# Kernel tuning notes

Hardware: AMD Instinct MI355X
Metric: run time of the kernel (lower is better)

Reference implementation:

```python
import jax, jax.numpy as jnp
import numpy as np

D = 1024
H = 16

def setup_inputs() -> dict:
    key = jax.random.key(0)
    ks = jax.random.split(key, 5)
    x = jax.random.normal(ks[0], (4, 2048, D), dtype=jnp.float32)
    lim = 1.0 / np.sqrt(D)
    W_qkv = jax.random.uniform(ks[1], (D, 3 * D), minval=-lim, maxval=lim, dtype=jnp.float32)
    b_qkv = jax.random.uniform(ks[2], (3 * D,), minval=-lim, maxval=lim, dtype=jnp.float32)
    W_proj = jax.random.uniform(ks[3], (D, D), minval=-lim, maxval=lim, dtype=jnp.float32)
    b_proj = jax.random.uniform(ks[4], (D,), minval=-lim, maxval=lim, dtype=jnp.float32)
    return {"x": x, "W_qkv": W_qkv, "b_qkv": b_qkv, "W_proj": W_proj, "b_proj": b_proj}

def reference(x, W_qkv, b_qkv, W_proj, b_proj):
    B, T, d = x.shape
    hd = d // H
    scale = hd ** (-0.5)
    qkv = x @ W_qkv + b_qkv                       # [B,T,3D]
    qkv = qkv.reshape(B, T, 3, H, hd)
    q = qkv[:, :, 0].transpose(0, 2, 1, 3)        # [B,H,T,hd]
    k = qkv[:, :, 1].transpose(0, 2, 1, 3)
    v = qkv[:, :, 2].transpose(0, 2, 1, 3)
    scores = jnp.einsum('bhqd,bhkd->bhqk', q, k) * scale
    attn = jax.nn.softmax(scores, axis=-1)
    y = jnp.einsum('bhqk,bhkd->bhqd', attn, v)    # [B,H,T,hd]
    y = y.transpose(0, 2, 1, 3).reshape(B, T, d)
    return y @ W_proj + b_proj
```

## Files before the change

### kernel.cpp

```cpp
#include <hip/hip_runtime.h>


typedef __attribute__((ext_vector_type(8))) short bf16x8;
typedef __attribute__((ext_vector_type(8))) unsigned short u16x8;
typedef __attribute__((ext_vector_type(4))) float f32x4;
typedef __attribute__((ext_vector_type(16))) float f32x16;

#define DEV static __device__ __forceinline__

DEV unsigned short f2b(float f) {
  union { float f; unsigned int i; } v; v.f = f;
  unsigned int x = v.i;
  return (unsigned short)((x + 0x7FFFu + ((x >> 16) & 1u)) >> 16);
}

DEV f32x4 mfma16(bf16x8 a, bf16x8 b, f32x4 c) {
  return __builtin_amdgcn_mfma_f32_16x16x32_bf16(a, b, c, 0, 0, 0);
}
DEV f32x16 mfma32(bf16x8 a, bf16x8 b, f32x16 c) {
  return __builtin_amdgcn_mfma_f32_32x32x16_bf16(a, b, c, 0, 0, 0);
}

DEV void gl_lds16(const unsigned short* g, unsigned short* l) {
  __builtin_amdgcn_global_load_lds(
      (const __attribute__((address_space(1))) unsigned int*)g,
      (__attribute__((address_space(3))) unsigned int*)l, 16, 0, 0);
}

DEV void pk_swap(float a0, float a1, float b0, float b1,
                 unsigned int& w_lo, unsigned int& w_hi) {
  unsigned int a, b;
  asm("v_cvt_pk_bf16_f32 %0, %1, %2" : "=v"(a) : "v"(a0), "v"(a1));
  asm("v_cvt_pk_bf16_f32 %0, %1, %2" : "=v"(b) : "v"(b0), "v"(b1));
  asm("v_permlane32_swap_b32 %0, %1" : "+v"(a), "+v"(b));
  w_lo = a; w_hi = b;
}

__global__ __launch_bounds__(256) void prep(
    const float* __restrict__ x, unsigned short* __restrict__ xbf,
    const float* __restrict__ Wqkv, unsigned short* __restrict__ WqkvT,
    const float* __restrict__ Wproj, unsigned short* __restrict__ WprojT) {
  const int bid = blockIdx.x;
  if (bid < 8192) {
    const int i = (bid * 256 + threadIdx.x) * 4;
    const float4 v = *(const float4*)(x + i);
    ushort4 o;
    o.x = f2b(v.x); o.y = f2b(v.y); o.z = f2b(v.z); o.w = f2b(v.w);
    *(ushort4*)(xbf + i) = o;
    return;
  }
  __shared__ float tile[32][33];
  const float* in; unsigned short* out; int C, bx, by;
  if (bid < 11264) {
    const int bb = bid - 8192;
    bx = bb % 96; by = bb / 96; in = Wqkv; out = WqkvT; C = 3072;
  } else {
    const int bb = bid - 11264;
    bx = bb % 32; by = bb / 32; in = Wproj; out = WprojT; C = 1024;
  }
  const int R = 1024;
  const int tx = threadIdx.x & 31, ty = threadIdx.x >> 5;
  const int c0 = bx * 32, r0 = by * 32;
#pragma unroll
  for (int i = 0; i < 32; i += 8)
    tile[ty + i][tx] = in[(size_t)(r0 + ty + i) * C + (c0 + tx)];
  __syncthreads();
#pragma unroll
  for (int i = 0; i < 32; i += 8)
    out[(size_t)(c0 + ty + i) * R + (r0 + tx)] = f2b(tile[tx][ty + i]);
}

#define QSCALE 0.18033688f
template <int MODE>
__global__ __launch_bounds__(256, 2) void gemm_bt(
    const unsigned short* __restrict__ A, const unsigned short* __restrict__ Bt,
    const float* __restrict__ bias, void* __restrict__ out_v,
    int M, int N, int K) {
  __shared__ __align__(16) unsigned short As[128 * 64];
  __shared__ __align__(16) unsigned short Bs[128 * 64];
  const int tid = threadIdx.x;
  const int w = tid >> 6, l = tid & 63, g = l >> 4, ln = l & 15;
  const int wm = (w & 1) * 64, wn = (w >> 1) * 64;

  const int nwg = gridDim.x * gridDim.y;
  int wg = blockIdx.y * gridDim.x + blockIdx.x;
  wg = (wg & 7) * (nwg >> 3) + (wg >> 3);
  const int m0 = (wg / gridDim.x) * 128, n0 = (wg % gridDim.x) * 128;

  f32x4 acc[4][4];
#pragma unroll
  for (int i = 0; i < 4; ++i)
#pragma unroll
    for (int j = 0; j < 4; ++j) acc[i][j] = (f32x4){0.f, 0.f, 0.f, 0.f};

  const unsigned short* Ab = A + (size_t)m0 * K;
  const unsigned short* Bb = Bt + (size_t)n0 * K;
  const int lx = ln & 7;

  for (int k0 = 0; k0 < K; k0 += 64) {
#pragma unroll
    for (int i = 0; i < 4; ++i) {
      const int ch = tid + i * 256;
      const int ar = ch >> 3, s = ch & 7;
      const int sc = (s ^ (ar & 7)) * 8;
      gl_lds16(Ab + (size_t)ar * K + k0 + sc, &As[ch * 8]);
      gl_lds16(Bb + (size_t)ar * K + k0 + sc, &Bs[ch * 8]);
    }
    __syncthreads();
#pragma unroll
    for (int ks = 0; ks < 2; ++ks) {
      const int so = ((ks * 4 + g) ^ lx) * 8;
      bf16x8 af[4], bf[4];
#pragma unroll
      for (int mi = 0; mi < 4; ++mi)
        af[mi] = *(const bf16x8*)&As[(wm + mi * 16 + ln) * 64 + so];
#pragma unroll
      for (int ni = 0; ni < 4; ++ni)
        bf[ni] = *(const bf16x8*)&Bs[(wn + ni * 16 + ln) * 64 + so];
#pragma unroll
      for (int mi = 0; mi < 4; ++mi)
#pragma unroll
        for (int ni = 0; ni < 4; ++ni)
          acc[mi][ni] = mfma16(af[mi], bf[ni], acc[mi][ni]);
    }
    __syncthreads();
  }

#pragma unroll
  for (int mi = 0; mi < 4; ++mi) {
#pragma unroll
    for (int ni = 0; ni < 4; ++ni) {
      const int row0 = m0 + wm + mi * 16 + 4 * g;
      const int col = n0 + wn + ni * 16 + ln;
      const float bv = bias[col];
      if (MODE == 0) {
        const int which = col >> 10;
        const int h = (col >> 6) & 15;
        const int dd = col & 63;
        const int b = row0 >> 11, t0 = row0 & 2047;
        if (which == 2) {
          unsigned short* dst = (unsigned short*)out_v + (size_t)3 * 8388608u;
          ushort4 o;
          o.x = f2b(acc[mi][ni][0] + bv);
          o.y = f2b(acc[mi][ni][1] + bv);
          o.z = f2b(acc[mi][ni][2] + bv);
          o.w = f2b(acc[mi][ni][3] + bv);
          *(ushort4*)&dst[(((size_t)(b * 16 + h)) * 64 + dd) * 2048 + t0] = o;
        } else {
          unsigned short* dst = (unsigned short*)out_v + (size_t)which * 8388608u;
#pragma unroll
          for (int r = 0; r < 4; ++r) {
            float v = acc[mi][ni][r] + bv;
            if (which == 0) v *= QSCALE;
            dst[(((size_t)(b * 16 + h)) * 2048 + t0 + r) * 64 + dd] = f2b(v);
          }
        }
      } else {
#pragma unroll
        for (int r = 0; r < 4; ++r)
          ((float*)out_v)[(size_t)(row0 + r) * N + col] = acc[mi][ni][r] + bv;
      }
    }
  }
}

__global__ __launch_bounds__(256, 2) void attn(
    const unsigned short* __restrict__ Q, const unsigned short* __restrict__ K,
    const unsigned short* __restrict__ Vtg, unsigned short* __restrict__ Y) {
  __shared__ __align__(16) unsigned short Qs[128 * 72];
  __shared__ __align__(16) unsigned short Ks[64 * 72];
  __shared__ __align__(16) unsigned short Vt[64 * 72];

  const int tid = threadIdx.x;
  const int w = tid >> 6, l = tid & 63;
  const int l32 = l & 31, lh = l >> 5;
  const int wg = blockIdx.y * 16 + blockIdx.x;
  const int swz = (wg & 7) * 128 + (wg >> 3);
  const int bh = swz >> 4;
  const int q0 = (swz & 15) * 128;

  const unsigned short* Qb = Q + (size_t)bh * 131072;
  const unsigned short* Kb = K + (size_t)bh * 131072;
  const unsigned short* Vb = Vtg + (size_t)bh * 131072;

#pragma unroll
  for (int i = 0; i < 4; ++i) {
    const int c = tid + i * 256;
    u16x8 v = *(const u16x8*)(Qb + (size_t)q0 * 64 + c * 8);
    *(u16x8*)&Qs[(c >> 3) * 72 + (c & 7) * 8] = v;
  }
  __syncthreads();
  bf16x8 aq[4];
#pragma unroll
  for (int kb = 0; kb < 4; ++kb)
    aq[kb] = *(const bf16x8*)&Qs[(w * 32 + l32) * 72 + kb * 16 + lh * 8];

  const short one_b = (short)0x3F80;
  const bf16x8 vones = (bf16x8){one_b, one_b, one_b, one_b,
                                one_b, one_b, one_b, one_b};

  f32x16 o[2], os;
#pragma unroll
  for (int db = 0; db < 2; ++db)
#pragma unroll
    for (int r = 0; r < 16; ++r) o[db][r] = 0.f;
#pragma unroll
  for (int r = 0; r < 16; ++r) os[r] = 0.f;

  for (int kt = 0; kt < 32; ++kt) {
#pragma unroll
    for (int i = 0; i < 2; ++i) {
      const int c = tid + i * 256;
      const int row = c >> 3, cc = (c & 7) * 8;
      u16x8 kv = *(const u16x8*)(Kb + (size_t)kt * 4096 + c * 8);
      u16x8 vv = *(const u16x8*)(Vb + (size_t)row * 2048 + kt * 64 + cc);
      *(u16x8*)&Ks[row * 72 + cc] = kv;
      *(u16x8*)&Vt[row * 72 + cc] = vv;
    }
    __syncthreads();

    f32x16 s[2];
#pragma unroll
    for (int nb = 0; nb < 2; ++nb) {
#pragma unroll
      for (int r = 0; r < 16; ++r) s[nb][r] = 0.f;
#pragma unroll
      for (int kb = 0; kb < 4; ++kb) {
        bf16x8 bk = *(const bf16x8*)&Ks[(nb * 32 + l32) * 72 + kb * 16 + lh * 8];
        s[nb] = mfma32(bk, aq[kb], s[nb]);
      }
    }

    bf16x8 ap[4];
#pragma unroll
    for (int nb = 0; nb < 2; ++nb) {
      float pe[16];
#pragma unroll
      for (int r = 0; r < 16; ++r)
        pe[r] = __builtin_amdgcn_exp2f(s[nb][r]);
      union { unsigned int wd[4]; bf16x8 v; } u0, u1;
      pk_swap(pe[0], pe[1], pe[4], pe[5], u0.wd[0], u0.wd[2]);
      pk_swap(pe[2], pe[3], pe[6], pe[7], u0.wd[1], u0.wd[3]);
      pk_swap(pe[8], pe[9], pe[12], pe[13], u1.wd[0], u1.wd[2]);
      pk_swap(pe[10], pe[11], pe[14], pe[15], u1.wd[1], u1.wd[3]);
      ap[2 * nb + 0] = u0.v;
      ap[2 * nb + 1] = u1.v;
    }

#pragma unroll
    for (int ks = 0; ks < 4; ++ks) {
      os = mfma32(ap[ks], vones, os);
#pragma unroll
      for (int db = 0; db < 2; ++db) {
        bf16x8 bv = *(const bf16x8*)&Vt[(db * 32 + l32) * 72 + ks * 16 + lh * 8];
        o[db] = mfma32(ap[ks], bv, o[db]);
      }
    }
    __syncthreads();
  }

  float iv[16];
#pragma unroll
  for (int r = 0; r < 16; ++r) iv[r] = 1.f / os[r];

  const int b = bh >> 4, h = bh & 15;
#pragma unroll
  for (int db = 0; db < 2; ++db)
#pragma unroll
    for (int r = 0; r < 16; ++r) {
      const int row = (r & 3) + 8 * (r >> 2) + 4 * lh;
      const int t = q0 + w * 32 + row;
      Y[(size_t)(b * 2048 + t) * 1024 + h * 64 + db * 32 + l32] =
          f2b(o[db][r] * iv[r]);
    }
}

extern "C" void kernel_launch(void* const* d_in, const int* in_sizes, int n_in,
                              void* d_out, int out_size, void* d_ws, size_t ws_size,
                              hipStream_t stream) {
  const float* x     = (const float*)d_in[0];
  const float* Wqkv  = (const float*)d_in[1];
  const float* bqkv  = (const float*)d_in[2];
  const float* Wproj = (const float*)d_in[3];
  const float* bproj = (const float*)d_in[4];
  float* out = (float*)d_out;
  unsigned short* ws = (unsigned short*)d_ws;

  unsigned short* xbf    = ws;
  unsigned short* Yw     = xbf;
  unsigned short* WqkvT  = xbf + 8388608;
  unsigned short* WprojT = WqkvT + 3072 * 1024;
  unsigned short* Qw     = WprojT + 1024 * 1024;
  unsigned short* Kw     = Qw + 8388608;
  unsigned short* Vw     = Kw + 8388608;
  unsigned short* Vtw    = Vw + 8388608;
  (void)Vw; (void)Kw;

  prep<<<12288, 256, 0, stream>>>(x, xbf, Wqkv, WqkvT, Wproj, WprojT);
  gemm_bt<0><<<dim3(24, 64), 256, 0, stream>>>(xbf, WqkvT, bqkv, Qw, 8192, 3072, 1024);
  attn<<<dim3(16, 64), 256, 0, stream>>>(Qw, Qw + 8388608, Vtw, Yw);
  gemm_bt<1><<<dim3(8, 64), 256, 0, stream>>>(Yw, WprojT, bproj, out, 8192, 1024, 1024);
}
```

Baseline: 253.0 us.

## Use 64-row tiles for projection GEMM and compute softmax row sums with VALU

```diff
diff --git a/kernel.cpp b/kernel.cpp
--- a/kernel.cpp
+++ b/kernel.cpp
@@ -71,10 +71,9 @@
 }
 
 #define QSCALE 0.18033688f
-template <int MODE>
-__global__ __launch_bounds__(256, 2) void gemm_bt(
+__global__ __launch_bounds__(256, 2) void gemm_qkv(
     const unsigned short* __restrict__ A, const unsigned short* __restrict__ Bt,
-    const float* __restrict__ bias, void* __restrict__ out_v,
+    const float* __restrict__ bias, unsigned short* __restrict__ out,
     int M, int N, int K) {
   __shared__ __align__(16) unsigned short As[128 * 64];
   __shared__ __align__(16) unsigned short Bs[128 * 64];
@@ -133,33 +132,101 @@
       const int row0 = m0 + wm + mi * 16 + 4 * g;
       const int col = n0 + wn + ni * 16 + ln;
       const float bv = bias[col];
-      if (MODE == 0) {
-        const int which = col >> 10;
-        const int h = (col >> 6) & 15;
-        const int dd = col & 63;
-        const int b = row0 >> 11, t0 = row0 & 2047;
-        if (which == 2) {
-          unsigned short* dst = (unsigned short*)out_v + (size_t)3 * 8388608u;
-          ushort4 o;
-          o.x = f2b(acc[mi][ni][0] + bv);
-          o.y = f2b(acc[mi][ni][1] + bv);
-          o.z = f2b(acc[mi][ni][2] + bv);
-          o.w = f2b(acc[mi][ni][3] + bv);
-          *(ushort4*)&dst[(((size_t)(b * 16 + h)) * 64 + dd) * 2048 + t0] = o;
-        } else {
-          unsigned short* dst = (unsigned short*)out_v + (size_t)which * 8388608u;
-#pragma unroll
-          for (int r = 0; r < 4; ++r) {
-            float v = acc[mi][ni][r] + bv;
-            if (which == 0) v *= QSCALE;
-            dst[(((size_t)(b * 16 + h)) * 2048 + t0 + r) * 64 + dd] = f2b(v);
-          }
+      const int which = col >> 10;
+      const int h = (col >> 6) & 15;
+      const int dd = col & 63;
+      const int b = row0 >> 11, t0 = row0 & 2047;
+      if (which == 2) {
+        unsigned short* dst = out + (size_t)3 * 8388608u;
+        ushort4 o;
+        o.x = f2b(acc[mi][ni][0] + bv);
+        o.y = f2b(acc[mi][ni][1] + bv);
+        o.z = f2b(acc[mi][ni][2] + bv);
+        o.w = f2b(acc[mi][ni][3] + bv);
+        *(ushort4*)&dst[(((size_t)(b * 16 + h)) * 64 + dd) * 2048 + t0] = o;
+      } else {
+        unsigned short* dst = out + (size_t)which * 8388608u;
+#pragma unroll
+        for (int r = 0; r < 4; ++r) {
+          float v = acc[mi][ni][r] + bv;
+          if (which == 0) v *= QSCALE;
+          dst[(((size_t)(b * 16 + h)) * 2048 + t0 + r) * 64 + dd] = f2b(v);
         }
-      } else {
-#pragma unroll
-        for (int r = 0; r < 4; ++r)
-          ((float*)out_v)[(size_t)(row0 + r) * N + col] = acc[mi][ni][r] + bv;
       }
+    }
+  }
+}
+
+__global__ __launch_bounds__(256, 2) void gemm_proj(
+    const unsigned short* __restrict__ A, const unsigned short* __restrict__ Bt,
+    const float* __restrict__ bias, float* __restrict__ out,
+    int M, int N, int K) {
+  __shared__ __align__(16) unsigned short As[64 * 64];
+  __shared__ __align__(16) unsigned short Bs[128 * 64];
+  const int tid = threadIdx.x;
+  const int w = tid >> 6, l = tid & 63, g = l >> 4, ln = l & 15;
+  const int wm = (w & 1) * 32, wn = (w >> 1) * 64;
+
+  const int nwg = gridDim.x * gridDim.y;
+  int wg = blockIdx.y * gridDim.x + blockIdx.x;
+  wg = (wg & 7) * (nwg >> 3) + (wg >> 3);
+  const int m0 = (wg / gridDim.x) * 64, n0 = (wg % gridDim.x) * 128;
+
+  f32x4 acc[2][4];
+#pragma unroll
+  for (int i = 0; i < 2; ++i)
+#pragma unroll
+    for (int j = 0; j < 4; ++j) acc[i][j] = (f32x4){0.f, 0.f, 0.f, 0.f};
+
+  const unsigned short* Ab = A + (size_t)m0 * K;
+  const unsigned short* Bb = Bt + (size_t)n0 * K;
+  const int lx = ln & 7;
+
+  for (int k0 = 0; k0 < K; k0 += 64) {
+#pragma unroll
+    for (int i = 0; i < 2; ++i) {
+      const int ch = tid + i * 256;
+      const int ar = ch >> 3, s = ch & 7;
+      const int sc = (s ^ (ar & 7)) * 8;
+      gl_lds16(Ab + (size_t)ar * K + k0 + sc, &As[ch * 8]);
+    }
+#pragma unroll
+    for (int i = 0; i < 4; ++i) {
+      const int ch = tid + i * 256;
+      const int br = ch >> 3, s = ch & 7;
+      const int sc = (s ^ (br & 7)) * 8;
+      gl_lds16(Bb + (size_t)br * K + k0 + sc, &Bs[ch * 8]);
+    }
+    __syncthreads();
+#pragma unroll
+    for (int ks = 0; ks < 2; ++ks) {
+      const int so = ((ks * 4 + g) ^ lx) * 8;
+      bf16x8 af[2], bf[4];
+#pragma unroll
+      for (int mi = 0; mi < 2; ++mi)
+        af[mi] = *(const bf16x8*)&As[(wm + mi * 16 + ln) * 64 + so];
+#pragma unroll
+      for (int ni = 0; ni < 4; ++ni)
+        bf[ni] = *(const bf16x8*)&Bs[(wn + ni * 16 + ln) * 64 + so];
+#pragma unroll
+      for (int mi = 0; mi < 2; ++mi)
+#pragma unroll
+        for (int ni = 0; ni < 4; ++ni)
+          acc[mi][ni] = mfma16(af[mi], bf[ni], acc[mi][ni]);
+    }
+    __syncthreads();
+  }
+
+#pragma unroll
+  for (int mi = 0; mi < 2; ++mi) {
+#pragma unroll
+    for (int ni = 0; ni < 4; ++ni) {
+      const int row0 = m0 + wm + mi * 16 + 4 * g;
+      const int col = n0 + wn + ni * 16 + ln;
+      const float bv = bias[col];
+#pragma unroll
+      for (int r = 0; r < 4; ++r)
+        out[(size_t)(row0 + r) * N + col] = acc[mi][ni][r] + bv;
     }
   }
 }
@@ -195,17 +262,12 @@
   for (int kb = 0; kb < 4; ++kb)
     aq[kb] = *(const bf16x8*)&Qs[(w * 32 + l32) * 72 + kb * 16 + lh * 8];
 
-  const short one_b = (short)0x3F80;
-  const bf16x8 vones = (bf16x8){one_b, one_b, one_b, one_b,
-                                one_b, one_b, one_b, one_b};
-
-  f32x16 o[2], os;
+  f32x16 o[2];
 #pragma unroll
   for (int db = 0; db < 2; ++db)
 #pragma unroll
     for (int r = 0; r < 16; ++r) o[db][r] = 0.f;
-#pragma unroll
-  for (int r = 0; r < 16; ++r) os[r] = 0.f;
+  float lsp[4] = {0.f, 0.f, 0.f, 0.f};
 
   for (int kt = 0; kt < 32; ++kt) {
 #pragma unroll
@@ -236,8 +298,10 @@
     for (int nb = 0; nb < 2; ++nb) {
       float pe[16];
 #pragma unroll
-      for (int r = 0; r < 16; ++r)
+      for (int r = 0; r < 16; ++r) {
         pe[r] = __builtin_amdgcn_exp2f(s[nb][r]);
+        lsp[r & 3] += pe[r];
+      }
       union { unsigned int wd[4]; bf16x8 v; } u0, u1;
       pk_swap(pe[0], pe[1], pe[4], pe[5], u0.wd[0], u0.wd[2]);
       pk_swap(pe[2], pe[3], pe[6], pe[7], u0.wd[1], u0.wd[3]);
@@ -248,20 +312,23 @@
     }
 
 #pragma unroll
-    for (int ks = 0; ks < 4; ++ks) {
-      os = mfma32(ap[ks], vones, os);
+    for (int ks = 0; ks < 4; ++ks)
 #pragma unroll
       for (int db = 0; db < 2; ++db) {
         bf16x8 bv = *(const bf16x8*)&Vt[(db * 32 + l32) * 72 + ks * 16 + lh * 8];
         o[db] = mfma32(ap[ks], bv, o[db]);
       }
-    }
-    __syncthreads();
-  }
-
+    __syncthreads();
+  }
+
+  float lsum = (lsp[0] + lsp[1]) + (lsp[2] + lsp[3]);
+  lsum += __shfl_xor(lsum, 32, 64);
   float iv[16];
 #pragma unroll
-  for (int r = 0; r < 16; ++r) iv[r] = 1.f / os[r];
+  for (int r = 0; r < 16; ++r) {
+    const int row = (r & 3) + 8 * (r >> 2) + 4 * lh;
+    iv[r] = 1.f / __shfl(lsum, row, 64);
+  }
 
   const int b = bh >> 4, h = bh & 15;
 #pragma unroll
@@ -294,10 +361,10 @@
   unsigned short* Kw     = Qw + 8388608;
   unsigned short* Vw     = Kw + 8388608;
   unsigned short* Vtw    = Vw + 8388608;
-  (void)Vw; (void)Kw;
+  (void)Vw;
 
   prep<<<12288, 256, 0, stream>>>(x, xbf, Wqkv, WqkvT, Wproj, WprojT);
-  gemm_bt<0><<<dim3(24, 64), 256, 0, stream>>>(xbf, WqkvT, bqkv, Qw, 8192, 3072, 1024);
-  attn<<<dim3(16, 64), 256, 0, stream>>>(Qw, Qw + 8388608, Vtw, Yw);
-  gemm_bt<1><<<dim3(8, 64), 256, 0, stream>>>(Yw, WprojT, bproj, out, 8192, 1024, 1024);
-}
+  gemm_qkv<<<dim3(24, 64), 256, 0, stream>>>(xbf, WqkvT, bqkv, Qw, 8192, 3072, 1024);
+  attn<<<dim3(16, 64), 256, 0, stream>>>(Qw, Kw, Vtw, Yw);
+  gemm_proj<<<dim3(8, 128), 256, 0, stream>>>(Yw, WprojT, bproj, out, 8192, 1024, 1024);
+}
```

Result: faster. 246.8 us (-2.5%).
